# Kernel optimization log

Hardware: AMD Instinct MI355X
Metric: run time of the kernel (lower is better)

## Reference

```python
import jax, jax.numpy as jnp
import numpy as np

L = 12      # n_layers
C = 768     # n_embd = dim = dim_att
H = 12      # heads
N = 64      # head_size_a
FF = 2688   # dim_ffn = int(768*3.5//32*32)
P = 2       # patch_size
INCH = 4
IMG = 32
NCLS = 1000
FREQ = 256
HC = C // 2  # conv stem channels (dim//2)
B = 32
D_MIX = 32
D_DEC = 64
LNX_EPS = 1e-5 * 8.0 ** 2  # GroupNorm eps with head_size_divisor=8


def _ln(x, w=None, b=None, eps=1e-5):
    m = x.mean(-1, keepdims=True)
    v = x.var(-1, keepdims=True)
    xh = (x - m) * jax.lax.rsqrt(v + eps)
    if w is not None:
        xh = xh * w + b
    return xh


def _shift(x):  # RWKV token shift: prepend zero row, drop last
    return jnp.pad(x, ((0, 0), (1, 0), (0, 0)))[:, :-1]


def _gn_img(x, w, b, groups=32, eps=1e-5):
    Bb, Ch, Hh, Ww = x.shape
    xg = x.reshape(Bb, groups, Ch // groups, Hh, Ww)
    m = xg.mean((2, 3, 4), keepdims=True)
    v = xg.var((2, 3, 4), keepdims=True)
    xg = (xg - m) * jax.lax.rsqrt(v + eps)
    return xg.reshape(Bb, Ch, Hh, Ww) * w[None, :, None, None] + b[None, :, None, None]


def _conv5(x, w, b):
    y = jax.lax.conv_general_dilated(x, w, (1, 1), ((2, 2), (2, 2)),
                                     dimension_numbers=('NCHW', 'OIHW', 'NCHW'))
    return y + b[None, :, None, None]


def _wkv(r, k, v, w, u):
    # r,k,v,w: (B,T,H,N); u: (H,N). S[b,h,i,j]: key i -> value j.
    def step(S, inp):
        rt, kt, vt, wt = inp  # each (B,H,N)
        kv = kt[..., :, None] * vt[..., None, :]           # (B,H,N,N)
        y = jnp.einsum('bhi,bhij->bhj', rt, S + u[None, :, :, None] * kv)
        S = wt[..., :, None] * S + kv
        return S, y
    S0 = jnp.zeros((r.shape[0], H, N, N), r.dtype)
    seq = tuple(jnp.moveaxis(a, 1, 0) for a in (r, k, v, w))
    _, ys = jax.lax.scan(step, S0, seq)
    return jnp.moveaxis(ys, 0, 1)  # (B,T,H,N)


def _timemix(x, p):
    Bb, Tt, _ = x.shape
    xx = _shift(x) - x
    xxx = x + xx * p['maa'][0]
    mix = jnp.tanh(xxx @ p['tm_w1']).reshape(Bb, Tt, 5, D_MIX)
    m = jnp.einsum('btfd,fdc->fbtc', mix, p['tm_w2'])  # (5,B,T,C): mw,mk,mv,mr,mg
    xw = x + xx * (p['maa'][1] + m[0])
    xk = x + xx * (p['maa'][2] + m[1])
    xv = x + xx * (p['maa'][3] + m[2])
    xr = x + xx * (p['maa'][4] + m[3])
    xg = x + xx * (p['maa'][5] + m[4])
    r = (xr @ p['r_w'].T).reshape(Bb, Tt, H, N)
    k = (xk @ p['k_w'].T).reshape(Bb, Tt, H, N)
    v = (xv @ p['v_w'].T).reshape(Bb, Tt, H, N)
    g = jax.nn.silu(xg @ p['g_w'].T)
    ww = p['td'] + jnp.tanh(xw @ p['td_w1']) @ p['td_w2']
    w = jnp.exp(-jnp.exp(ww)).reshape(Bb, Tt, H, N)
    y = _wkv(r, k, v, w, p['faaaa'])  # (B,T,H,N)
    mn = y.mean(-1, keepdims=True)
    vr = y.var(-1, keepdims=True)
    y = ((y - mn) * jax.lax.rsqrt(vr + LNX_EPS)).reshape(Bb, Tt, C) * p['lnx_w'] + p['lnx_b']
    return (y * g) @ p['o_w'].T


def _chanmix(x, p):
    xx = _shift(x) - x
    xk = x + xx * p['fmaa'][0]
    xr = x + xx * p['fmaa'][1]
    k = jnp.square(jax.nn.relu(xk @ p['fk_w'].T))
    return jax.nn.sigmoid(xr @ p['fr_w'].T) * (k @ p['fv_w'].T)


def _forward(x, t, y, c1_w, c1_b, gn1_w, gn1_b, c2_w, c2_b, gn2_w, gn2_b,
             xe_w, xe_b, te_w1, te_b1, te_w2, te_b2, y_tab, ln0_w, ln0_b,
             ln1_w, ln1_b, ln2_w, ln2_b, att_maa, tm_w1, tm_w2, td, td_w1,
             td_w2, faaaa, r_w, k_w, v_w, o_w, g_w, lnx_w, lnx_b, ffn_maa,
             fk_w, fr_w, fv_w, ada_w, ada_b, fl_ada_w, fl_ada_b, fl_w, fl_b):
    Bb = x.shape[0]
    h = jax.nn.silu(_conv5(x, c1_w, c1_b))
    h = _gn_img(h, gn1_w, gn1_b)
    h = jax.nn.silu(_conv5(h, c2_w, c2_b))
    h = _gn_img(h, gn2_w, gn2_b)
    # patchify: (B,HC,IMG,IMG) -> (B,T,P*P*HC)
    G = IMG // P
    h = h.reshape(Bb, HC, G, P, G, P).transpose(0, 2, 4, 1, 3, 5).reshape(Bb, G * G, HC * P * P)
    xs = h @ xe_w.T + xe_b
    # timestep embedding
    half = FREQ // 2
    freqs = jnp.exp(-jnp.log(10000.0) * jnp.arange(half, dtype=jnp.float32) / half)
    ang = t[:, None] * freqs[None]
    temb = jnp.concatenate([jnp.cos(ang), jnp.sin(ang)], -1)
    temb = jax.nn.silu(temb @ te_w1.T + te_b1) @ te_w2.T + te_b2
    c = temb + y_tab[y]  # adaln_input (B,C)
    for l in range(L):
        ada = jax.nn.silu(c) @ ada_w[l].T + ada_b[l]
        sm, scm, gm, sp, scp, gp = jnp.split(ada, 6, axis=1)
        if l == 0:
            xs = _ln(xs, ln0_w, ln0_b)
        p = dict(maa=att_maa[l], tm_w1=tm_w1[l], tm_w2=tm_w2[l], td=td[l],
                 td_w1=td_w1[l], td_w2=td_w2[l], faaaa=faaaa[l], r_w=r_w[l],
                 k_w=k_w[l], v_w=v_w[l], o_w=o_w[l], g_w=g_w[l], lnx_w=lnx_w[l],
                 lnx_b=lnx_b[l], fmaa=ffn_maa[l], fk_w=fk_w[l], fr_w=fr_w[l],
                 fv_w=fv_w[l])
        hmod = _ln(xs, ln1_w[l], ln1_b[l]) * (1 + scm[:, None, :]) + sm[:, None, :]
        xs = xs + gm[:, None, :] * _timemix(hmod, p)
        hmod = _ln(xs, ln2_w[l], ln2_b[l]) * (1 + scp[:, None, :]) + sp[:, None, :]
        xs = xs + gp[:, None, :] * _chanmix(hmod, p)
    ada = jax.nn.silu(c) @ fl_ada_w.T + fl_ada_b
    sh, sc = jnp.split(ada, 2, axis=1)
    out = (_ln(xs, eps=1e-6) * (1 + sc[:, None, :]) + sh[:, None, :]) @ fl_w.T + fl_b
    G = IMG // P
    out = out.reshape(Bb, G, G, P, P, INCH)
    out = jnp.einsum('nhwpqc->nchpwq', out).reshape(Bb, INCH, IMG, IMG)
    return out


def setup_inputs() -> dict:
    key = jax.random.key(0)
    ks = iter(jax.random.split(key, 64))
    def rn(shape, s=0.02):
        return (jax.random.normal(next(ks), shape) * s).astype(jnp.float32)
    inp = {}
    inp['x'] = jax.random.normal(next(ks), (B, INCH, IMG, IMG), jnp.float32)
    inp['t'] = jax.random.uniform(next(ks), (B,), jnp.float32) * 1000.0
    inp['y'] = jax.random.randint(next(ks), (B,), 0, NCLS)
    inp['c1_w'] = rn((HC, INCH, 5, 5), 0.05); inp['c1_b'] = jnp.zeros(HC)
    inp['gn1_w'] = jnp.ones(HC); inp['gn1_b'] = jnp.zeros(HC)
    inp['c2_w'] = rn((HC, HC, 5, 5), 0.02); inp['c2_b'] = jnp.zeros(HC)
    inp['gn2_w'] = jnp.ones(HC); inp['gn2_b'] = jnp.zeros(HC)
    inp['xe_w'] = rn((C, P * P * HC)); inp['xe_b'] = jnp.zeros(C)
    inp['te_w1'] = rn((C, FREQ)); inp['te_b1'] = jnp.zeros(C)
    inp['te_w2'] = rn((C, C)); inp['te_b2'] = jnp.zeros(C)
    inp['y_tab'] = rn((NCLS + 1, C))
    inp['ln0_w'] = jnp.ones(C); inp['ln0_b'] = jnp.zeros(C)
    inp['ln1_w'] = jnp.ones((L, C)); inp['ln1_b'] = jnp.zeros((L, C))
    inp['ln2_w'] = jnp.ones((L, C)); inp['ln2_b'] = jnp.zeros((L, C))
    inp['att_maa'] = jax.random.uniform(next(ks), (L, 6, C), jnp.float32)
    inp['tm_w1'] = rn((L, C, 5 * D_MIX), 0.01)
    inp['tm_w2'] = rn((L, 5, D_MIX, C), 0.01)
    inp['td'] = rn((L, C), 0.5) - 3.0
    inp['td_w1'] = rn((L, C, D_DEC), 0.01)
    inp['td_w2'] = rn((L, D_DEC, C), 0.01)
    inp['faaaa'] = rn((L, H, N), 0.1)
    for nm in ('r_w', 'k_w', 'v_w', 'o_w', 'g_w'):
        inp[nm] = rn((L, C, C))
    inp['lnx_w'] = jnp.ones((L, C)); inp['lnx_b'] = jnp.zeros((L, C))
    inp['ffn_maa'] = jax.random.uniform(next(ks), (L, 2, C), jnp.float32)
    inp['fk_w'] = rn((L, FF, C)); inp['fr_w'] = rn((L, C, C)); inp['fv_w'] = rn((L, C, FF))
    inp['ada_w'] = rn((L, 6 * C, C)); inp['ada_b'] = jnp.zeros((L, 6 * C))
    inp['fl_ada_w'] = rn((2 * C, C)); inp['fl_ada_b'] = jnp.zeros(2 * C)
    inp['fl_w'] = rn((P * P * INCH, C)); inp['fl_b'] = jnp.zeros(P * P * INCH)
    return inp


def reference(x, t, y, c1_w, c1_b, gn1_w, gn1_b, c2_w, c2_b, gn2_w, gn2_b,
              xe_w, xe_b, te_w1, te_b1, te_w2, te_b2, y_tab, ln0_w, ln0_b,
              ln1_w, ln1_b, ln2_w, ln2_b, att_maa, tm_w1, tm_w2, td, td_w1,
              td_w2, faaaa, r_w, k_w, v_w, o_w, g_w, lnx_w, lnx_b, ffn_maa,
              fk_w, fr_w, fv_w, ada_w, ada_b, fl_ada_w, fl_ada_b, fl_w, fl_b):
    return _forward(x, t, y, c1_w, c1_b, gn1_w, gn1_b, c2_w, c2_b, gn2_w, gn2_b,
                    xe_w, xe_b, te_w1, te_b1, te_w2, te_b2, y_tab, ln0_w, ln0_b,
                    ln1_w, ln1_b, ln2_w, ln2_b, att_maa, tm_w1, tm_w2, td, td_w1,
                    td_w2, faaaa, r_w, k_w, v_w, o_w, g_w, lnx_w, lnx_b, ffn_maa,
                    fk_w, fr_w, fv_w, ada_w, ada_b, fl_ada_w, fl_ada_b, fl_w, fl_b)
```

## Files before the change

kernel.cpp:

```cpp
#include <hip/hip_runtime.h>
#include <math.h>


typedef short  s16x8 __attribute__((ext_vector_type(8)));
typedef float  f32x4 __attribute__((ext_vector_type(4)));
typedef __attribute__((address_space(1))) const void as1_cv;
typedef __attribute__((address_space(3))) void as3_v;

#define GLDS16(gp, lp) __builtin_amdgcn_global_load_lds( \
    (as1_cv*)(unsigned long long)(const void*)(gp), \
    (as3_v*)(unsigned int)(unsigned long long)(void*)(lp), 16, 0, 0)

static __device__ __forceinline__ float sigf(float x){ return 1.f/(1.f+expf(-x)); }
static __device__ __forceinline__ unsigned short f2b(float x){
  unsigned int u = __builtin_bit_cast(unsigned int, x);
  unsigned int r = (u + 0x7FFFu + ((u >> 16) & 1u)) >> 16;
  return (unsigned short)r;
}
static __device__ __forceinline__ float b2f(unsigned short h){
  unsigned int u = ((unsigned int)h)<<16; return __builtin_bit_cast(float,u);
}

static const size_t O_XS    = 0ull;
static const size_t O_HMOD  = 6291456ull;
// ... 106 lines not shown
template<int EPI>
__global__ __launch_bounds__(256) void bgemm_k(
    const unsigned short* __restrict__ A, const unsigned short* __restrict__ B,
    void* __restrict__ Cv, const float* __restrict__ bias,
    const float* __restrict__ p1, const void* __restrict__ p2, int pstride,
    int M, int N, int K)
{
  __shared__ __align__(16) unsigned short As[128][64];
  __shared__ __align__(16) unsigned short Bs[128][64];
  const int tid = threadIdx.x;
  const int w = tid >> 6, lane = tid & 63;
  const int row0 = blockIdx.y * 128, col0 = blockIdx.x * 128;
  const int wr = w >> 1, wc = w & 1;
  const int l15 = lane & 15, l4 = lane >> 4;
  const int kkc = ((lane & 7) ^ (lane >> 3)) * 8;
  f32x4 acc[4][4] = {};
  for (int k0 = 0; k0 < K; k0 += 64) {
    #pragma unroll
    for (int i = 0; i < 4; i++) {
      const int rb = i*32 + w*8;
      const int r  = rb + (lane >> 3);
      GLDS16(A + (size_t)(row0 + r)*K + k0 + kkc, &As[rb][0]);
      GLDS16(B + (size_t)(col0 + r)*K + k0 + kkc, &Bs[rb][0]);
    }
    __syncthreads();
    #pragma unroll
    for (int ks = 0; ks < 2; ks++) {
      s16x8 af[4], bf[4];
      #pragma unroll
      for (int m = 0; m < 4; m++) {
        const int r = wr*64 + m*16 + l15;
        const int sl = (ks*4 + l4) ^ (r & 7);
        af[m] = *reinterpret_cast<const s16x8*>(&As[r][sl*8]);
      }
      #pragma unroll
      for (int n = 0; n < 4; n++) {
        const int r = wc*64 + n*16 + l15;
        const int sl = (ks*4 + l4) ^ (r & 7);
        bf[n] = *reinterpret_cast<const s16x8*>(&Bs[r][sl*8]);
      }
      #pragma unroll
      for (int m = 0; m < 4; m++)
        #pragma unroll
        for (int n = 0; n < 4; n++)
          acc[m][n] = __builtin_amdgcn_mfma_f32_16x16x32_bf16(af[m], bf[n], acc[m][n], 0, 0, 0);
    }
    __syncthreads();
  }
  float* Cf = (float*)Cv; unsigned short* Ch = (unsigned short*)Cv;
  const unsigned short* p2h = (const unsigned short*)p2;
  #pragma unroll
  for (int m = 0; m < 4; m++) {
    const int rbase = row0 + wr*64 + m*16 + (l4<<2);
    #pragma unroll
    for (int n = 0; n < 4; n++) {
      const int c = col0 + wc*64 + n*16 + l15;
      if (c >= N) continue;
      #pragma unroll
      for (int q = 0; q < 4; q++) {
        const int r = rbase + q;
        const int bb = r >> 8;
        float v = acc[m][n][q];
        const size_t idx = (size_t)r*N + c;
        if (EPI==BEPI_F32)            Cf[idx] = v;
        else if (EPI==BEPI_BIAS_F32)  Cf[idx] = v + bias[c];
        else if (EPI==BEPI_SILU_F32)  Cf[idx] = v*sigf(v);
        else if (EPI==BEPI_SIG_F32)   Cf[idx] = sigf(v);
        else if (EPI==BEPI_RELU2_BF16){ float t=fmaxf(v,0.f); Ch[idx] = f2b(t*t); }
        else if (EPI==BEPI_RES_GM)    Cf[idx] += p1[(size_t)bb*pstride + c]*v;
        else if (EPI==BEPI_RES_GP16)  Cf[idx] += p1[(size_t)bb*pstride + c]*(b2f(p2h[idx])*v);
        else if (EPI==BEPI_TANH_BF16) Ch[idx] = f2b(tanhf(v));
        else if (EPI==BEPI_WDEC_F32)  Cf[idx] = expf(-expf(v + p1[c]));
      }
    }
  }
}

#define BGEMM(EPI,A16,B16,Cp,bias,p1,p2,ps,M,N,K) \
  bgemm_k<EPI><<<dim3(((N)+127)/128,(M)/128),dim3(256),0,stream>>>( \
    (const unsigned short*)(A16),(const unsigned short*)(B16),(void*)(Cp),(bias),(p1),(p2),(ps),(M),(N),(K))

struct BGrp { const unsigned short* A; const unsigned short* B; void* C;
              int epi; int N; int gx; };
struct BGrp5 { BGrp g[5]; };

__global__ __launch_bounds__(256) void bgemm_grp_k(BGrp5 G, int M, int K)
{
  const BGrp gr = G.g[blockIdx.z];
  if ((int)blockIdx.x >= gr.gx) return;
  __shared__ __align__(16) unsigned short As[128][64];
  __shared__ __align__(16) unsigned short Bs[128][64];
  const int tid = threadIdx.x;
  const int w = tid >> 6, lane = tid & 63;
  const int row0 = blockIdx.y * 128, col0 = blockIdx.x * 128;
  const int wr = w >> 1, wc = w & 1;
  const int l15 = lane & 15, l4 = lane >> 4;
  const int kkc = ((lane & 7) ^ (lane >> 3)) * 8;
  const int N = gr.N;
  f32x4 acc[4][4] = {};
  for (int k0 = 0; k0 < K; k0 += 64) {
    #pragma unroll
    for (int i = 0; i < 4; i++) {
      const int rb = i*32 + w*8;
      const int r  = rb + (lane >> 3);
      GLDS16(gr.A + (size_t)(row0 + r)*K + k0 + kkc, &As[rb][0]);
      GLDS16(gr.B + (size_t)(col0 + r)*K + k0 + kkc, &Bs[rb][0]);
    }
    __syncthreads();
    #pragma unroll
    for (int ks = 0; ks < 2; ks++) {
      s16x8 af[4], bf[4];
      #pragma unroll
      for (int m = 0; m < 4; m++) {
        const int r = wr*64 + m*16 + l15;
        const int sl = (ks*4 + l4) ^ (r & 7);
        af[m] = *reinterpret_cast<const s16x8*>(&As[r][sl*8]);
      }
      #pragma unroll
      for (int n = 0; n < 4; n++) {
        const int r = wc*64 + n*16 + l15;
        const int sl = (ks*4 + l4) ^ (r & 7);
        bf[n] = *reinterpret_cast<const s16x8*>(&Bs[r][sl*8]);
      }
      #pragma unroll
      for (int m = 0; m < 4; m++)
        #pragma unroll
        for (int n = 0; n < 4; n++)
          acc[m][n] = __builtin_amdgcn_mfma_f32_16x16x32_bf16(af[m], bf[n], acc[m][n], 0, 0, 0);
    }
    __syncthreads();
  }
  float* Cf = (float*)gr.C; unsigned short* Ch = (unsigned short*)gr.C;
  #pragma unroll
  for (int m = 0; m < 4; m++) {
    const int rbase = row0 + wr*64 + m*16 + (l4<<2);
    #pragma unroll
    for (int n = 0; n < 4; n++) {
      const int c = col0 + wc*64 + n*16 + l15;
      #pragma unroll
      for (int q = 0; q < 4; q++) {
        const int r = rbase + q;
        float v = acc[m][n][q];
        const size_t idx = (size_t)r*N + c;
        switch (gr.epi) {
          case 0: Cf[idx] = v; break;
          case 1: Cf[idx] = v*sigf(v); break;
          case 3: { float t=fmaxf(v,0.f); Ch[idx] = f2b(t*t); } break;
          case 4: Ch[idx] = f2b(v); break;
          case 5: Ch[idx] = f2b(v*sigf(v)); break;
          case 6: Ch[idx] = f2b(tanhf(v)); break;
          default: Ch[idx] = f2b(sigf(v)); break;
        }
      }
    }
  }
}

__global__ __launch_bounds__(256) void conv1_k(
    const float* __restrict__ x, const float* __restrict__ w,
    const float* __restrict__ bias, float* __restrict__ out)
{
  const int blk = blockIdx.x; const int bb = blk / 384; const int oc = blk % 384;
  __shared__ __align__(16) float sIn[4*1296];
  __shared__ __align__(16) float sW[100];
  const int tid = threadIdx.x;
  for (int idx=tid; idx<4*1296; idx+=256){
    int ic = idx/1296; int rem = idx - ic*1296;
    int yy = rem/36, xx = rem - yy*36;
    int gy = yy-2, gx = xx-2;
    float v = 0.f;
    if ((unsigned)gy < 32u && (unsigned)gx < 32u)
      v = x[(((size_t)bb*4+ic)*32+gy)*32+gx];
    sIn[idx]=v;
  }
  if (tid < 100) sW[tid] = w[(size_t)oc*100 + tid];
  __syncthreads();
  const float bv = bias[oc];
  #pragma unroll
  for (int i=0;i<4;i++){
    int p = tid + 256*i; int py=p>>5, px=p&31;
    int pb = py*36+px;
    float acc = bv;
    #pragma unroll
    for (int ic=0;ic<4;ic++)
      #pragma unroll
      for (int ky=0;ky<5;ky++)
        #pragma unroll
        for (int kx=0;kx<5;kx++)
          acc = fmaf(sIn[ic*1296 + pb + ky*36+kx], sW[ic*25+ky*5+kx], acc);
    out[((size_t)(bb*384+oc))*1024 + p] = acc*sigf(acc);
  }
}

__global__ __launch_bounds__(256) void gn_stats_nchw_k(
    const float* __restrict__ h, float* __restrict__ stats)
{
  const int blk = blockIdx.x;
  const size_t base = (size_t)blk*12288;
  const int tid = threadIdx.x;
  float s=0.f, s2=0.f;
  for (int idx=tid; idx<12288; idx+=256){ float v=h[base+idx]; s+=v; s2=fmaf(v,v,s2); }
  #pragma unroll
  for (int mask=32; mask>=1; mask>>=1){ s += __shfl_xor(s,mask); s2 += __shfl_xor(s2,mask); }
  __shared__ float ps[8];
  if ((tid&63)==0){ ps[tid>>6]=s; ps[4+(tid>>6)]=s2; }
  __syncthreads();
  if (tid==0){
    s = ps[0]+ps[1]+ps[2]+ps[3]; s2 = ps[4]+ps[5]+ps[6]+ps[7];
    float mean = s*(1.f/12288.f);
    float var  = s2*(1.f/12288.f) - mean*mean;
    stats[blk*2] = mean; stats[blk*2+1] = rsqrtf(var + 1e-5f);
  }
}

__global__ void zero16_k(unsigned short* __restrict__ p)
{
  size_t i = ((size_t)blockIdx.x*256 + threadIdx.x)*8;
  *reinterpret_cast<uint4*>(p + i) = make_uint4(0u,0u,0u,0u);
}

__global__ __launch_bounds__(256) void pad_apply_k(
    const float* __restrict__ img1, const float* __restrict__ stats,
    const float* __restrict__ w, const float* __restrict__ bgn,
    unsigned short* __restrict__ pad)
{
  __shared__ float t[8][33];
  const int b = blockIdx.x >> 5, y = blockIdx.x & 31;
  const int tid = threadIdx.x;
  for (int ic0 = 0; ic0 < 384; ic0 += 8) {
    const int icr = tid >> 5, xr = tid & 31;
    t[icr][xr] = img1[(((size_t)b*384 + ic0+icr)*32 + y)*32 + xr];
    __syncthreads();
    const int xw_ = tid >> 3, icw = tid & 7;
// ... 107 lines not shown
  if ((tid&63)==0){ ps[tid>>6]=s; ps[4+(tid>>6)]=s2; }
  __syncthreads();
  if (tid==0){
    s = ps[0]+ps[1]+ps[2]+ps[3]; s2 = ps[4]+ps[5]+ps[6]+ps[7];
    float mean = s*(1.f/12288.f);
    float var  = s2*(1.f/12288.f) - mean*mean;
    stats[(b*32+g)*2] = mean; stats[(b*32+g)*2+1] = rsqrtf(var + 1e-5f);
  }
}

__global__ void patchify_gn_k(const unsigned short* __restrict__ h, const float* __restrict__ stats,
                              const float* __restrict__ w, const float* __restrict__ bgn,
                              unsigned short* __restrict__ pm)
{
  int idx = blockIdx.x*256 + threadIdx.x;
  int row = idx/1536, f = idx - row*1536;
  int c = f>>2; int p=(f>>1)&1; int q=f&1;
  int bb=row>>8; int tok=row&255; int gh=tok>>4, gw=tok&15;
  int pix = (gh*2+p)*32 + gw*2+q;
  int g = c / 12;
  float mean = stats[(bb*32+g)*2], rstd = stats[(bb*32+g)*2+1];
  float v = (b2f(h[((size_t)bb*1024 + pix)*384 + c]) - mean)*rstd*w[c] + bgn[c];
  pm[idx] = f2b(v);
}

__global__ void temb_in_k(const float* __restrict__ t, float* __restrict__ out)
{
  int bb = blockIdx.x; int i = threadIdx.x;
  float fr = expf(-logf(10000.f) * (float)i / 128.f);
  float ang = t[bb]*fr;
  out[bb*256+i]     = cosf(ang);
  out[bb*256+128+i] = sinf(ang);
}

__global__ void siluc_k(const float* __restrict__ t2, const float* __restrict__ ytab,
                        const int* __restrict__ y, float* __restrict__ sc)
{
  int bb = blockIdx.x; int tid = threadIdx.x;
  int cls = y[bb];
  for (int c=tid; c<768; c+=256){
    float v = t2[bb*768+c] + ytab[(size_t)cls*768+c];
    sc[bb*768+c] = v*sigf(v);
  }
}

__global__ __launch_bounds__(256) void ln_mod_k(
    const float* __restrict__ in, float* __restrict__ out,
    const float* __restrict__ w, const float* __restrict__ b,
    const float* __restrict__ mod, int mstride, int sh_off, int sc_off, float eps)
{
  const int m = blockIdx.x; const int tid = threadIdx.x;
  const size_t base = (size_t)m*768;
  float v0=in[base+tid], v1=in[base+tid+256], v2=in[base+tid+512];
  float s = v0+v1+v2;
  float s2 = fmaf(v0,v0,fmaf(v1,v1,v2*v2));
  #pragma unroll
  for (int mask=32; mask>=1; mask>>=1){ s += __shfl_xor(s,mask); s2 += __shfl_xor(s2,mask); }
  __shared__ float ps[8];
  if ((tid&63)==0){ ps[tid>>6]=s; ps[4+(tid>>6)]=s2; }
  __syncthreads();
  s = ps[0]+ps[1]+ps[2]+ps[3]; s2 = ps[4]+ps[5]+ps[6]+ps[7];
  const float mean = s*(1.f/768.f);
  const float var  = s2*(1.f/768.f) - mean*mean;
  const float rstd = rsqrtf(var + eps);
  const int bb = m >> 8;
  #pragma unroll
  for (int k=0;k<3;k++){
    const int c = tid + k*256;
    float v = (k==0)?v0:((k==1)?v1:v2);
    float xh = (v-mean)*rstd;
    if (w) xh = fmaf(xh, w[c], b[c]);
    if (mod){
      float scv = mod[(size_t)bb*mstride + sc_off + c];
      float shv = mod[(size_t)bb*mstride + sh_off + c];
      xh = fmaf(xh, 1.f+scv, shv);
    }
    out[base+c] = xh;
  }
}

__global__ __launch_bounds__(256) void ln_shift_tm_k(
    const float* __restrict__ xs, const float* __restrict__ w, const float* __restrict__ b,
    const float* __restrict__ mod, const float* __restrict__ maa0,
    float* __restrict__ hmod, float* __restrict__ xx, unsigned short* __restrict__ xxx16)
{
  const int m = blockIdx.x, tid = threadIdx.x;
  const size_t base = (size_t)m*768;
  const int t = m & 255, bb = m >> 8;
  float c0=xs[base+tid], c1=xs[base+tid+256], c2=xs[base+tid+512];
  float p0=0.f,p1=0.f,p2=0.f;
  if (t) { p0=xs[base-768+tid]; p1=xs[base-512+tid]; p2=xs[base-256+tid]; }
  float sc_=c0+c1+c2, sc2=fmaf(c0,c0,fmaf(c1,c1,c2*c2));
  float sp_=p0+p1+p2, sp2=fmaf(p0,p0,fmaf(p1,p1,p2*p2));
  #pragma unroll
  for (int mask=32; mask>=1; mask>>=1){
    sc_+=__shfl_xor(sc_,mask); sc2+=__shfl_xor(sc2,mask);
    sp_+=__shfl_xor(sp_,mask); sp2+=__shfl_xor(sp2,mask);
  }
  __shared__ float ps[16];
  if ((tid&63)==0){ int wv=tid>>6; ps[wv]=sc_; ps[4+wv]=sc2; ps[8+wv]=sp_; ps[12+wv]=sp2; }
  __syncthreads();
  sc_=ps[0]+ps[1]+ps[2]+ps[3]; sc2=ps[4]+ps[5]+ps[6]+ps[7];
  sp_=ps[8]+ps[9]+ps[10]+ps[11]; sp2=ps[12]+ps[13]+ps[14]+ps[15];
  const float mc = sc_*(1.f/768.f), rc = rsqrtf(sc2*(1.f/768.f)-mc*mc + 1e-5f);
  const float mp = sp_*(1.f/768.f), rp = rsqrtf(sp2*(1.f/768.f)-mp*mp + 1e-5f);
  #pragma unroll
  for (int k=0;k<3;k++){
    const int c = tid + k*256;
    const float scv = mod[(size_t)bb*55296 + 768 + c];
    const float shv = mod[(size_t)bb*55296 + c];
    float cv = (k==0)?c0:((k==1)?c1:c2);
    float h = fmaf((cv-mc)*rc, w[c], b[c]);
    h = fmaf(h, 1.f+scv, shv);
    float pv = 0.f;
    if (t) {
      float pk = (k==0)?p0:((k==1)?p1:p2);
      pv = fmaf((pk-mp)*rp, w[c], b[c]);
      pv = fmaf(pv, 1.f+scv, shv);
    }
    const float d = pv - h;
    hmod[base+c] = h;
    xx[base+c] = d;
    xxx16[base+c] = f2b(fmaf(d, maa0[c], h));
  }
}

__global__ __launch_bounds__(256) void ln_shift_cm_k(
    const float* __restrict__ xs, const float* __restrict__ w, const float* __restrict__ b,
    const float* __restrict__ mod, const float* __restrict__ fmaa,
    unsigned short* __restrict__ xk16, unsigned short* __restrict__ xr16)
{
  const int m = blockIdx.x, tid = threadIdx.x;
  const size_t base = (size_t)m*768;
  const int t = m & 255, bb = m >> 8;
  float c0=xs[base+tid], c1=xs[base+tid+256], c2=xs[base+tid+512];
  float p0=0.f,p1=0.f,p2=0.f;
  if (t) { p0=xs[base-768+tid]; p1=xs[base-512+tid]; p2=xs[base-256+tid]; }
  float sc_=c0+c1+c2, sc2=fmaf(c0,c0,fmaf(c1,c1,c2*c2));
  float sp_=p0+p1+p2, sp2=fmaf(p0,p0,fmaf(p1,p1,p2*p2));
  #pragma unroll
  for (int mask=32; mask>=1; mask>>=1){
    sc_+=__shfl_xor(sc_,mask); sc2+=__shfl_xor(sc2,mask);
    sp_+=__shfl_xor(sp_,mask); sp2+=__shfl_xor(sp2,mask);
  }
  __shared__ float ps[16];
  if ((tid&63)==0){ int wv=tid>>6; ps[wv]=sc_; ps[4+wv]=sc2; ps[8+wv]=sp_; ps[12+wv]=sp2; }
  __syncthreads();
  sc_=ps[0]+ps[1]+ps[2]+ps[3]; sc2=ps[4]+ps[5]+ps[6]+ps[7];
  sp_=ps[8]+ps[9]+ps[10]+ps[11]; sp2=ps[12]+ps[13]+ps[14]+ps[15];
  const float mc = sc_*(1.f/768.f), rc = rsqrtf(sc2*(1.f/768.f)-mc*mc + 1e-5f);
  const float mp = sp_*(1.f/768.f), rp = rsqrtf(sp2*(1.f/768.f)-mp*mp + 1e-5f);
  #pragma unroll
  for (int k=0;k<3;k++){
    const int c = tid + k*256;
    const float scv = mod[(size_t)bb*55296 + 3072 + c];
    const float shv = mod[(size_t)bb*55296 + 2304 + c];
    float cv = (k==0)?c0:((k==1)?c1:c2);
    float h = fmaf((cv-mc)*rc, w[c], b[c]);
    h = fmaf(h, 1.f+scv, shv);
    float pv = 0.f;
    if (t) {
      float pk = (k==0)?p0:((k==1)?p1:p2);
      pv = fmaf((pk-mp)*rp, w[c], b[c]);
      pv = fmaf(pv, 1.f+scv, shv);
    }
    const float d = pv - h;
    xk16[base+c] = f2b(fmaf(d, fmaa[c], h));
    xr16[base+c] = f2b(fmaf(d, fmaa[768+c], h));
  }
}

__global__ __launch_bounds__(256) void five_mix_k(
    const unsigned short* __restrict__ mix16, const float* __restrict__ w2,
    const float* __restrict__ hmod, const float* __restrict__ xx,
    const float* __restrict__ maa15,
    unsigned short* __restrict__ xw, unsigned short* __restrict__ xk,
    unsigned short* __restrict__ xv, unsigned short* __restrict__ xr,
    unsigned short* __restrict__ xg)
{
  __shared__ __align__(16) float smix[8][160];
  const int m0 = blockIdx.x * 8;
  const int tid = threadIdx.x;
  for (int idx=tid; idx<8*160; idx+=256){
    int r = idx/160, d = idx - r*160;
    smix[r][d] = b2f(mix16[(size_t)(m0+r)*160 + d]);
  }
  __syncthreads();
  #pragma unroll 1
  for (int cc=0; cc<3; cc++){
    const int c = tid + cc*256;
    float hv[8], xv_[8];
    #pragma unroll
    for (int r=0;r<8;r++){ size_t id=(size_t)(m0+r)*768+c; hv[r]=hmod[id]; xv_[r]=xx[id]; }
    #pragma unroll 1
    for (int f=0; f<5; f++){
      float acc[8];
      const float base = maa15[f*768 + c];
      #pragma unroll
      for (int r=0;r<8;r++) acc[r]=base;
      #pragma unroll 1
      for (int d4=0; d4<8; d4++){
        float wv[4];
        #pragma unroll
        for (int q=0;q<4;q++) wv[q] = w2[(size_t)(f*32+d4*4+q)*768 + c];
        #pragma unroll
        for (int r=0;r<8;r++){
          const float4 mv = *reinterpret_cast<const float4*>(&smix[r][f*32+d4*4]);
          acc[r] = fmaf(mv.x,wv[0],fmaf(mv.y,wv[1],fmaf(mv.z,wv[2],fmaf(mv.w,wv[3],acc[r]))));
        }
      }
      #pragma unroll
      for (int r=0;r<8;r++){
        float val = fmaf(xv_[r], acc[r], hv[r]);
        size_t id = (size_t)(m0+r)*768+c;
        if (f==0) xw[id]=f2b(val);
        else if (f==1) xk[id]=f2b(val);
        else if (f==2) xv[id]=f2b(val);
        else if (f==3) xr[id]=f2b(val);
        else           xg[id]=f2b(val);
      }
    }
  }
}

__global__ __launch_bounds__(256) void wkv_k(
    const unsigned short* __restrict__ rg, const unsigned short* __restrict__ kg,
    const unsigned short* __restrict__ vg, const float* __restrict__ wg,
    const unsigned short* __restrict__ gg, const float* __restrict__ u,
    const float* __restrict__ lnxw, const float* __restrict__ lnxb,
    unsigned short* __restrict__ out16)
{
  const int bh = blockIdx.x; const int b = bh/12, h = bh%12;
  const int tid = threadIdx.x;
  const int w = tid >> 6, lane = tid & 63;
  const int l4 = lane >> 4, l15 = lane & 15;
  __shared__ __align__(16) unsigned short r16s[32][64], k16s[32][64], v16s[32][64], g16s[32][64];
  __shared__ __align__(16) float wds[32][64];
  __shared__ __align__(16) float Wl[33][64];
  __shared__ __align__(16) unsigned short rr16[32][64], kk16[32][64];
  __shared__ __align__(16) unsigned short kk2T[64][32], vT[64][32];
  __shared__ __align__(16) unsigned short S16T[64][64];
  __shared__ __align__(16) unsigned short A16[32][32];
  __shared__ float diag[32], ypsum[32][4], ypsq[32][4];

  reinterpret_cast<uint4*>(&S16T[0][0])[tid] = make_uint4(0,0,0,0);
  reinterpret_cast<uint4*>(&S16T[0][0])[256+tid] = make_uint4(0,0,0,0);

  const float u_lane = u[h*64 + lane];
  const int jj = w*16 + l15;
  const float lw = lnxw[h*64 + jj], lb = lnxb[h*64 + jj];
  const size_t gb = (size_t)(b*256)*768 + h*64;

  const int st_t = tid >> 3, st_i = (tid & 7) * 8;
  uint4 pr, pk, pv, pg; float4 pw0, pw1;

#define WKV_LOADC(c_) { \
    const size_t tb = gb + (size_t)((c_)*32 + st_t)*768 + st_i; \
    pr = *reinterpret_cast<const uint4*>(rg + tb); \
    pk = *reinterpret_cast<const uint4*>(kg + tb); \
    pv = *reinterpret_cast<const uint4*>(vg + tb); \
    pg = *reinterpret_cast<const uint4*>(gg + tb); \
    pw0 = *reinterpret_cast<const float4*>(wg + tb); \
    pw1 = *reinterpret_cast<const float4*>(wg + tb + 4); }
#define WKV_STAGE() { \
    *reinterpret_cast<uint4*>(&r16s[st_t][st_i]) = pr; \
    *reinterpret_cast<uint4*>(&k16s[st_t][st_i]) = pk; \
    *reinterpret_cast<uint4*>(&v16s[st_t][st_i]) = pv; \
    *reinterpret_cast<uint4*>(&g16s[st_t][st_i]) = pg; \
    *reinterpret_cast<float4*>(&wds[st_t][st_i]) = pw0; \
    *reinterpret_cast<float4*>(&wds[st_t][st_i+4]) = pw1; }

  f32x4 S_acc[4] = {};

  WKV_LOADC(0);
  WKV_STAGE();
  __syncthreads();

  #pragma unroll 1
  for (int c = 0; c < 8; ++c) {
    if (w == 0) {
      float wv[32];
      #pragma unroll
      for (int t=0;t<32;t++) wv[t] = wds[t][lane];
      float P = 1.f;
      Wl[0][lane] = 1.f;
      #pragma unroll
      for (int t=0;t<32;t++){ P *= wv[t]; Wl[t+1][lane] = P; }
    }
    __syncthreads();
    {
      const int t = st_t, i0 = st_i;
      s16x8 rv = *reinterpret_cast<const s16x8*>(&r16s[t][i0]);
      s16x8 kv = *reinterpret_cast<const s16x8*>(&k16s[t][i0]);
      s16x8 vv = *reinterpret_cast<const s16x8*>(&v16s[t][i0]);
      float4 wa0 = *reinterpret_cast<const float4*>(&Wl[t][i0]);
// ... 97 lines not shown
    #pragma unroll
    for (int m=0;m<2;m++)
      #pragma unroll
      for (int q=0;q<4;q++){
        float s1 = Y[m][q], s2 = s1*s1;
        #pragma unroll
        for (int mask=8; mask>=1; mask>>=1){ s1 += __shfl_xor(s1,mask); s2 += __shfl_xor(s2,mask); }
        if (l15==0){ const int t = m*16 + l4*4 + q; ypsum[t][w]=s1; ypsq[t][w]=s2; }
      }
    __syncthreads();
    #pragma unroll
    for (int m=0;m<2;m++)
      #pragma unroll
      for (int q=0;q<4;q++){
        const int t = m*16 + l4*4 + q;
        float s1 = ypsum[t][0]+ypsum[t][1]+ypsum[t][2]+ypsum[t][3];
        float s2 = ypsq[t][0]+ypsq[t][1]+ypsq[t][2]+ypsq[t][3];
        float mean = s1*(1.f/64.f);
        float var  = s2*(1.f/64.f) - mean*mean;
        float xh = (Y[m][q]-mean)*rsqrtf(var + 6.4e-4f);
        float o = fmaf(xh, lw, lb) * b2f(g16s[t][jj]);
        out16[gb + (size_t)(c*32+t)*768 + jj] = f2b(o);
      }
    if (c < 7) {
      __syncthreads();
      WKV_STAGE();
      __syncthreads();
    }
  }
#undef WKV_LOADC
#undef WKV_STAGE
}

__global__ void unpatch_k(const float* __restrict__ po, float* __restrict__ out)
{
  int idx = blockIdx.x*256 + threadIdx.x;
  int xq=idx&31; int yy=(idx>>5)&31; int ch=(idx>>10)&3; int bb=idx>>12;
  int gh=yy>>1, p=yy&1, gw=xq>>1, q=xq&1;
  out[idx] = po[((size_t)(bb*256+gh*16+gw))*16 + p*8+q*4+ch];
}

__global__ void f2b_k(const float* __restrict__ s, unsigned short* __restrict__ d)
{
  size_t i = ((size_t)blockIdx.x*256 + threadIdx.x)*8;
  float4 a = *reinterpret_cast<const float4*>(s+i);
  float4 b = *reinterpret_cast<const float4*>(s+i+4);
  s16x8 o;
  o[0]=(short)f2b(a.x); o[1]=(short)f2b(a.y); o[2]=(short)f2b(a.z); o[3]=(short)f2b(a.w);
  o[4]=(short)f2b(b.x); o[5]=(short)f2b(b.y); o[6]=(short)f2b(b.z); o[7]=(short)f2b(b.w);
  *reinterpret_cast<s16x8*>(d + i) = o;
}

__global__ void f2bw_layer_k(
    const float* __restrict__ r_, const float* __restrict__ k_, const float* __restrict__ v_,
    const float* __restrict__ o_, const float* __restrict__ g_, const float* __restrict__ fr_,
    const float* __restrict__ fk_, const float* __restrict__ fv_,
    const float* __restrict__ tm1, const float* __restrict__ td1, const float* __restrict__ td2,
    unsigned short* __restrict__ dst)
{
  if (blockIdx.x < 3744) {
    size_t i = ((size_t)blockIdx.x*256 + threadIdx.x)*8;
    const float* s; size_t off;
    if (i < 3538944) {
      unsigned seg = (unsigned)(i / 589824u); off = i - (size_t)seg*589824u;
      s = seg==0?r_:seg==1?k_:seg==2?v_:seg==3?o_:seg==4?g_:fr_;
    } else if (i < 5603328) { s = fk_; off = i - 3538944; }
    else                    { s = fv_; off = i - 5603328; }
    float4 a = *reinterpret_cast<const float4*>(s+off);
    float4 b = *reinterpret_cast<const float4*>(s+off+4);
    s16x8 o;
    o[0]=(short)f2b(a.x); o[1]=(short)f2b(a.y); o[2]=(short)f2b(a.z); o[3]=(short)f2b(a.w);
    o[4]=(short)f2b(b.x); o[5]=(short)f2b(b.y); o[6]=(short)f2b(b.z); o[7]=(short)f2b(b.w);
    *reinterpret_cast<s16x8*>(dst + i) = o;
  } else {
    int idx = (blockIdx.x-3744)*256 + threadIdx.x;
    unsigned short* rp = dst + 7667712;
    if (idx < 196608) {
      int n = idx/768, k = idx - n*768;
      rp[idx] = (n<160) ? f2b(tm1[(size_t)k*160 + n]) : (unsigned short)0;
    } else if (idx < 294912) {
      int i = idx-196608; int n = i/768, k = i - n*768;
      rp[idx] = (n<64) ? f2b(td1[(size_t)k*64 + n]) : (unsigned short)0;
    } else {
      int i = idx-294912; int n = i/128, kk = i & 127;
      rp[idx] = (kk<64) ? f2b(td2[(size_t)kk*768 + n]) : (unsigned short)0;
    }
  }
}

extern "C" void kernel_launch(void* const* d_in, const int* in_sizes, int n_in,
                              void* d_out, int out_size, void* d_ws, size_t ws_size,
                              hipStream_t stream)
{
  const float* x_in  = (const float*)d_in[0];
  const float* t_in  = (const float*)d_in[1];
  const int*   y_in  = (const int*)  d_in[2];
  const float* c1w   = (const float*)d_in[3];
  const float* c1b   = (const float*)d_in[4];
  const float* gn1w  = (const float*)d_in[5];
  const float* gn1b  = (const float*)d_in[6];
  const float* c2w   = (const float*)d_in[7];
  const float* c2b   = (const float*)d_in[8];
  const float* gn2w  = (const float*)d_in[9];
  const float* gn2b  = (const float*)d_in[10];
  const float* xew   = (const float*)d_in[11];
  const float* xeb   = (const float*)d_in[12];
  const float* tew1  = (const float*)d_in[13];
  const float* teb1  = (const float*)d_in[14];
  const float* tew2  = (const float*)d_in[15];
  const float* teb2  = (const float*)d_in[16];
  const float* ytab  = (const float*)d_in[17];
  const float* ln0w  = (const float*)d_in[18];
  const float* ln0b  = (const float*)d_in[19];
  const float* ln1w  = (const float*)d_in[20];
  const float* ln1b  = (const float*)d_in[21];
  const float* ln2w  = (const float*)d_in[22];
  const float* ln2b  = (const float*)d_in[23];
  const float* amaa  = (const float*)d_in[24];
  const float* tmw1  = (const float*)d_in[25];
  const float* tmw2  = (const float*)d_in[26];
  const float* tdv   = (const float*)d_in[27];
  const float* tdw1  = (const float*)d_in[28];
  const float* tdw2  = (const float*)d_in[29];
  const float* faa   = (const float*)d_in[30];
  const float* rw    = (const float*)d_in[31];
  const float* kw    = (const float*)d_in[32];
  const float* vw    = (const float*)d_in[33];
  const float* ow    = (const float*)d_in[34];
  const float* gw    = (const float*)d_in[35];
  const float* lnxw  = (const float*)d_in[36];
  const float* lnxb  = (const float*)d_in[37];
  const float* fmaa  = (const float*)d_in[38];
  const float* fkw   = (const float*)d_in[39];
  const float* frw   = (const float*)d_in[40];
  const float* fvw   = (const float*)d_in[41];
  const float* adaw  = (const float*)d_in[42];
  const float* adab  = (const float*)d_in[43];
  const float* flaw  = (const float*)d_in[44];
  const float* flab  = (const float*)d_in[45];
  const float* flw   = (const float*)d_in[46];
  const float* flb   = (const float*)d_in[47];

  float* Wf = (float*)d_ws;
  float* xs   = Wf+O_XS;   float* hmod = Wf+O_HMOD;
  float* ada  = Wf+O_ADA;  float* fla  = Wf+O_FLA;
  float* t2   = Wf+O_T2;   float* sc   = Wf+O_SC;
  float* ti   = Wf+O_TI;   float* t1   = Wf+O_T1;
  float* st1  = Wf+O_ST1;  float* st2  = Wf+O_ST2;
  unsigned short* xew16 = (unsigned short*)(Wf+O_XEW16);
  unsigned short* wl16  = (unsigned short*)(Wf+O_WL16);
  float* big = Wf+O_BIG;
  float* xxb  = big+L_XX;
  float* wd   = big+L_WD;
  unsigned short* rb16  = (unsigned short*)(big+L_XXX);
  unsigned short* kb16  = (unsigned short*)(big+L_KB);
  unsigned short* vb16  = (unsigned short*)(big+L_VB);
  unsigned short* gb16  = (unsigned short*)(big+L_GB);
  unsigned short* xw16  = (unsigned short*)(big+L_XW);
  unsigned short* xxx16 = (unsigned short*)(big+L_XXX);
  unsigned short* mixb16= (unsigned short*)(big+L_MIXB);
  unsigned short* wt16  = (unsigned short*)(big+L_WT);
  unsigned short* xk16 = (unsigned short*)(big+L_XK16);
  unsigned short* xv16 = (unsigned short*)(big+L_XV16);
  unsigned short* xr16 = (unsigned short*)(big+L_XR16);
  unsigned short* xg16 = (unsigned short*)(big+L_XG16);
  unsigned short* gnh16 = (unsigned short*)(big+L_GNH16);
  unsigned short* kbig16 = (unsigned short*)(big+L_KBIG16);
  float* img1 = big+S_IMG1;
  unsigned short* img2_16 = (unsigned short*)(big+S_IMG2);
  unsigned short* pad16  = (unsigned short*)(big+S_PAD16);
  unsigned short* wtap16 = (unsigned short*)(big+S_WTAP16);
  unsigned short* pm16   = (unsigned short*)(big+S_PM16);
  float* pout = big+L_MIXB;
  unsigned short* dr  = wl16;
  unsigned short* dk  = wl16 + 589824;
  unsigned short* dv  = wl16 + 1179648;
  unsigned short* do_ = wl16 + 1769472;
  unsigned short* dg  = wl16 + 2359296;
  unsigned short* dfr = wl16 + 2949120;
  unsigned short* dfk = wl16 + 3538944;
  unsigned short* dfv = wl16 + 5603328;
  unsigned short* dtm1t = wl16 + 7667712;
  unsigned short* dtd1t = wl16 + 7864320;
  unsigned short* dtd2t = wl16 + 7962624;

  conv1_k<<<dim3(32*384),dim3(256),0,stream>>>(x_in, c1w, c1b, img1);
  gn_stats_nchw_k<<<dim3(1024),dim3(256),0,stream>>>(img1, st1);
  zero16_k<<<dim3(7776),dim3(256),0,stream>>>(pad16);
  pad_apply_k<<<dim3(1024),dim3(256),0,stream>>>(img1, st1, gn1w, gn1b, pad16);
  wrepack_k<<<dim3(384),dim3(256),0,stream>>>(c2w, wtap16);
  conv2m_k<<<dim3(768),dim3(256),0,stream>>>(pad16, wtap16, c2b, img2_16);
  gn_stats_nhwc_k<<<dim3(1024),dim3(256),0,stream>>>(img2_16, st2);
  patchify_gn_k<<<dim3(49152),dim3(256),0,stream>>>(img2_16, st2, gn2w, gn2b, pm16);
  f2b_k<<<dim3(576),dim3(256),0,stream>>>(xew, xew16);
  BGEMM(BEPI_BIAS_F32, pm16, xew16, xs, xeb, nullptr,nullptr,0, 8192,768,1536);

  temb_in_k<<<dim3(32),dim3(128),0,stream>>>(t_in, ti);
  GEMM(EPI_SILU,true, ti, tew1, t1, teb1, 32,768,256);
  GEMM(EPI_NONE,true, t1, tew2, t2, teb2, 32,768,768);
  siluc_k<<<dim3(32),dim3(256),0,stream>>>(t2, ytab, y_in, sc);
  GEMM(EPI_NONE,true, sc, adaw, ada, adab, 32,55296,768);
  GEMM(EPI_NONE,true, sc, flaw, fla, flab, 32,1536,768);

  ln_mod_k<<<dim3(8192),dim3(256),0,stream>>>(xs, xs, ln0w, ln0b, nullptr, 0,0,0, 1e-5f);

  for (int l=0; l<12; l++){
    const float* adal = ada + (size_t)l*4608;
    f2bw_layer_k<<<dim3(5280),dim3(256),0,stream>>>(
        rw+(size_t)l*589824, kw+(size_t)l*589824, vw+(size_t)l*589824,
        ow+(size_t)l*589824, gw+(size_t)l*589824, frw+(size_t)l*589824,
        fkw+(size_t)l*2064384, fvw+(size_t)l*2064384,
        tmw1+(size_t)l*122880, tdw1+(size_t)l*49152, tdw2+(size_t)l*49152, wl16);
    ln_shift_tm_k<<<dim3(8192),dim3(256),0,stream>>>(
        xs, ln1w+(size_t)l*768, ln1b+(size_t)l*768, adal, amaa+(size_t)l*4608,
        hmod, xxb, xxx16);
    BGEMM(BEPI_TANH_BF16, xxx16, dtm1t, mixb16, nullptr,nullptr,nullptr,0, 8192,160,768);
    five_mix_k<<<dim3(1024),dim3(256),0,stream>>>(mixb16, tmw2+(size_t)l*122880, hmod, xxb,
                                                  amaa+(size_t)l*4608+768, xw16,xk16,xv16,xr16,xg16);
    {
      BGrp5 G;
      G.g[0].A=xr16; G.g[0].B=dr;    G.g[0].C=rb16; G.g[0].epi=4; G.g[0].N=768; G.g[0].gx=6;
      G.g[1].A=xk16; G.g[1].B=dk;    G.g[1].C=kb16; G.g[1].epi=4; G.g[1].N=768; G.g[1].gx=6;
      G.g[2].A=xv16; G.g[2].B=dv;    G.g[2].C=vb16; G.g[2].epi=4; G.g[2].N=768; G.g[2].gx=6;
      G.g[3].A=xg16; G.g[3].B=dg;    G.g[3].C=gb16; G.g[3].epi=5; G.g[3].N=768; G.g[3].gx=6;
      G.g[4].A=xw16; G.g[4].B=dtd1t; G.g[4].C=wt16; G.g[4].epi=6; G.g[4].N=128; G.g[4].gx=1;
      bgemm_grp_k<<<dim3(6,64,5),dim3(256),0,stream>>>(G, 8192, 768);
    }
    BGEMM(BEPI_WDEC_F32, wt16, dtd2t, wd, nullptr, tdv+(size_t)l*768, nullptr,0, 8192,768,128);
    wkv_k<<<dim3(384),dim3(256),0,stream>>>(rb16, kb16, vb16, wd, gb16, faa+(size_t)l*768,
                                            lnxw+(size_t)l*768, lnxb+(size_t)l*768, gnh16);
    BGEMM(BEPI_RES_GM, gnh16, do_, xs, nullptr, adal+1536, nullptr, 55296, 8192,768,768);
    ln_shift_cm_k<<<dim3(8192),dim3(256),0,stream>>>(
        xs, ln2w+(size_t)l*768, ln2b+(size_t)l*768, adal, fmaa+(size_t)l*1536, xk16, xr16);
    {
      BGrp5 G;
      G.g[0].A=xk16; G.g[0].B=dfk; G.g[0].C=kbig16; G.g[0].epi=3; G.g[0].N=2688; G.g[0].gx=21;
      G.g[1].A=xr16; G.g[1].B=dfr; G.g[1].C=gb16;   G.g[1].epi=7; G.g[1].N=768;  G.g[1].gx=6;
      G.g[2]=G.g[1]; G.g[3]=G.g[1]; G.g[4]=G.g[1];
      bgemm_grp_k<<<dim3(21,64,2),dim3(256),0,stream>>>(G, 8192, 768);
    }
    BGEMM(BEPI_RES_GP16, kbig16, dfv, xs, nullptr, adal+3840, gb16, 55296, 8192,768,2688);
  }

  ln_mod_k<<<dim3(8192),dim3(256),0,stream>>>(xs, hmod, nullptr, nullptr, fla, 1536, 0, 768, 1e-6f);
  GEMM(EPI_NONE,true, hmod, flw, pout, flb, 8192,16,768);
  unpatch_k<<<dim3(512),dim3(256),0,stream>>>(pout, (float*)d_out);
}
```

Measured before the change: 9.043 ms.

## Store timemix intermediates as bf16 and split decay LoRA out of grouped GEMM

hmod and xx are now written and read in bf16 instead of fp32, roughly halving their memory traffic between ln_shift_tm_k and five_mix_k. five_mix_k processes 16 rows per block instead of 8, so each w2 weight load is reused across more rows. The decay LoRA first GEMM is removed from the grouped projection GEMM and run as a standalone N=64 GEMM, and its second stage now uses K=64 instead of a zero-padded 128, which shrinks the repacked weights and the f2bw grid. The bf16 intermediates lower precision, and the larger per-thread register arrays may reduce occupancy.

```diff
diff --git a/kernel.cpp b/kernel.cpp
--- a/kernel.cpp
+++ b/kernel.cpp
@@ -212,9 +212,9 @@
 
 struct BGrp { const unsigned short* A; const unsigned short* B; void* C;
               int epi; int N; int gx; };
-struct BGrp5 { BGrp g[5]; };
-
-__global__ __launch_bounds__(256) void bgemm_grp_k(BGrp5 G, int M, int K)
+struct BGrp4 { BGrp g[4]; };
+
+__global__ __launch_bounds__(256) void bgemm_grp_k(BGrp4 G, int M, int K)
 {
   const BGrp gr = G.g[blockIdx.z];
   if ((int)blockIdx.x >= gr.gx) return;
@@ -278,7 +278,6 @@
           case 3: { float t=fmaxf(v,0.f); Ch[idx] = f2b(t*t); } break;
           case 4: Ch[idx] = f2b(v); break;
           case 5: Ch[idx] = f2b(v*sigf(v)); break;
-          case 6: Ch[idx] = f2b(tanhf(v)); break;
           default: Ch[idx] = f2b(sigf(v)); break;
         }
       }
@@ -552,7 +551,8 @@
 __global__ __launch_bounds__(256) void ln_shift_tm_k(
     const float* __restrict__ xs, const float* __restrict__ w, const float* __restrict__ b,
     const float* __restrict__ mod, const float* __restrict__ maa0,
-    float* __restrict__ hmod, float* __restrict__ xx, unsigned short* __restrict__ xxx16)
+    unsigned short* __restrict__ hmod16, unsigned short* __restrict__ xx16,
+    unsigned short* __restrict__ xxx16)
 {
   const int m = blockIdx.x, tid = threadIdx.x;
   const size_t base = (size_t)m*768;
@@ -589,8 +589,8 @@
       pv = fmaf(pv, 1.f+scv, shv);
     }
     const float d = pv - h;
-    hmod[base+c] = h;
-    xx[base+c] = d;
+    hmod16[base+c] = f2b(h);
+    xx16[base+c] = f2b(d);
     xxx16[base+c] = f2b(fmaf(d, maa0[c], h));
   }
 }
@@ -642,16 +642,16 @@
 
 __global__ __launch_bounds__(256) void five_mix_k(
     const unsigned short* __restrict__ mix16, const float* __restrict__ w2,
-    const float* __restrict__ hmod, const float* __restrict__ xx,
+    const unsigned short* __restrict__ hmod16, const unsigned short* __restrict__ xx16,
     const float* __restrict__ maa15,
     unsigned short* __restrict__ xw, unsigned short* __restrict__ xk,
     unsigned short* __restrict__ xv, unsigned short* __restrict__ xr,
     unsigned short* __restrict__ xg)
 {
-  __shared__ __align__(16) float smix[8][160];
-  const int m0 = blockIdx.x * 8;
+  __shared__ __align__(16) float smix[16][160];
+  const int m0 = blockIdx.x * 16;
   const int tid = threadIdx.x;
-  for (int idx=tid; idx<8*160; idx+=256){
+  for (int idx=tid; idx<16*160; idx+=256){
     int r = idx/160, d = idx - r*160;
     smix[r][d] = b2f(mix16[(size_t)(m0+r)*160 + d]);
   }
@@ -659,28 +659,31 @@
   #pragma unroll 1
   for (int cc=0; cc<3; cc++){
     const int c = tid + cc*256;
-    float hv[8], xv_[8];
-    #pragma unroll
-    for (int r=0;r<8;r++){ size_t id=(size_t)(m0+r)*768+c; hv[r]=hmod[id]; xv_[r]=xx[id]; }
+    float hv[16], xv_[16];
+    #pragma unroll
+    for (int r=0;r<16;r++){
+      size_t id=(size_t)(m0+r)*768+c;
+      hv[r]=b2f(hmod16[id]); xv_[r]=b2f(xx16[id]);
+    }
     #pragma unroll 1
     for (int f=0; f<5; f++){
-      float acc[8];
+      float acc[16];
       const float base = maa15[f*768 + c];
       #pragma unroll
-      for (int r=0;r<8;r++) acc[r]=base;
+      for (int r=0;r<16;r++) acc[r]=base;
       #pragma unroll 1
       for (int d4=0; d4<8; d4++){
         float wv[4];
         #pragma unroll
         for (int q=0;q<4;q++) wv[q] = w2[(size_t)(f*32+d4*4+q)*768 + c];
         #pragma unroll
-        for (int r=0;r<8;r++){
+        for (int r=0;r<16;r++){
           const float4 mv = *reinterpret_cast<const float4*>(&smix[r][f*32+d4*4]);
           acc[r] = fmaf(mv.x,wv[0],fmaf(mv.y,wv[1],fmaf(mv.z,wv[2],fmaf(mv.w,wv[3],acc[r]))));
         }
       }
       #pragma unroll
-      for (int r=0;r<8;r++){
+      for (int r=0;r<16;r++){
         float val = fmaf(xv_[r], acc[r], hv[r]);
         size_t id = (size_t)(m0+r)*768+c;
         if (f==0) xw[id]=f2b(val);
@@ -944,8 +947,8 @@
       int i = idx-196608; int n = i/768, k = i - n*768;
       rp[idx] = (n<64) ? f2b(td1[(size_t)k*64 + n]) : (unsigned short)0;
     } else {
-      int i = idx-294912; int n = i/128, kk = i & 127;
-      rp[idx] = (kk<64) ? f2b(td2[(size_t)kk*768 + n]) : (unsigned short)0;
+      int i = idx-294912; int n = i/64, k = i - n*64;
+      rp[idx] = f2b(td2[(size_t)k*768 + n]);
     }
   }
 }
@@ -1004,16 +1007,17 @@
   const float* flb   = (const float*)d_in[47];
 
   float* Wf = (float*)d_ws;
-  float* xs   = Wf+O_XS;   float* hmod = Wf+O_HMOD;
+  float* xs   = Wf+O_XS;   float* hmodf = Wf+O_HMOD;
   float* ada  = Wf+O_ADA;  float* fla  = Wf+O_FLA;
   float* t2   = Wf+O_T2;   float* sc   = Wf+O_SC;
   float* ti   = Wf+O_TI;   float* t1   = Wf+O_T1;
   float* st1  = Wf+O_ST1;  float* st2  = Wf+O_ST2;
   unsigned short* xew16 = (unsigned short*)(Wf+O_XEW16);
   unsigned short* wl16  = (unsigned short*)(Wf+O_WL16);
+  unsigned short* hmod16 = (unsigned short*)(Wf+O_HMOD);
   float* big = Wf+O_BIG;
-  float* xxb  = big+L_XX;
   float* wd   = big+L_WD;
+  unsigned short* xx16  = (unsigned short*)(big+L_XX);
   unsigned short* rb16  = (unsigned short*)(big+L_XXX);
   unsigned short* kb16  = (unsigned short*)(big+L_KB);
   unsigned short* vb16  = (unsigned short*)(big+L_VB);
@@ -1068,43 +1072,43 @@
 
   for (int l=0; l<12; l++){
     const float* adal = ada + (size_t)l*4608;
-    f2bw_layer_k<<<dim3(5280),dim3(256),0,stream>>>(
+    f2bw_layer_k<<<dim3(5088),dim3(256),0,stream>>>(
         rw+(size_t)l*589824, kw+(size_t)l*589824, vw+(size_t)l*589824,
         ow+(size_t)l*589824, gw+(size_t)l*589824, frw+(size_t)l*589824,
         fkw+(size_t)l*2064384, fvw+(size_t)l*2064384,
         tmw1+(size_t)l*122880, tdw1+(size_t)l*49152, tdw2+(size_t)l*49152, wl16);
     ln_shift_tm_k<<<dim3(8192),dim3(256),0,stream>>>(
         xs, ln1w+(size_t)l*768, ln1b+(size_t)l*768, adal, amaa+(size_t)l*4608,
-        hmod, xxb, xxx16);
+        hmod16, xx16, xxx16);
     BGEMM(BEPI_TANH_BF16, xxx16, dtm1t, mixb16, nullptr,nullptr,nullptr,0, 8192,160,768);
-    five_mix_k<<<dim3(1024),dim3(256),0,stream>>>(mixb16, tmw2+(size_t)l*122880, hmod, xxb,
-                                                  amaa+(size_t)l*4608+768, xw16,xk16,xv16,xr16,xg16);
+    five_mix_k<<<dim3(512),dim3(256),0,stream>>>(mixb16, tmw2+(size_t)l*122880, hmod16, xx16,
+                                                 amaa+(size_t)l*4608+768, xw16,xk16,xv16,xr16,xg16);
+    BGEMM(BEPI_TANH_BF16, xw16, dtd1t, wt16, nullptr,nullptr,nullptr,0, 8192,64,768);
+    BGEMM(BEPI_WDEC_F32, wt16, dtd2t, wd, nullptr, tdv+(size_t)l*768, nullptr,0, 8192,768,64);
     {
-      BGrp5 G;
-      G.g[0].A=xr16; G.g[0].B=dr;    G.g[0].C=rb16; G.g[0].epi=4; G.g[0].N=768; G.g[0].gx=6;
-      G.g[1].A=xk16; G.g[1].B=dk;    G.g[1].C=kb16; G.g[1].epi=4; G.g[1].N=768; G.g[1].gx=6;
-      G.g[2].A=xv16; G.g[2].B=dv;    G.g[2].C=vb16; G.g[2].epi=4; G.g[2].N=768; G.g[2].gx=6;
-      G.g[3].A=xg16; G.g[3].B=dg;    G.g[3].C=gb16; G.g[3].epi=5; G.g[3].N=768; G.g[3].gx=6;
-      G.g[4].A=xw16; G.g[4].B=dtd1t; G.g[4].C=wt16; G.g[4].epi=6; G.g[4].N=128; G.g[4].gx=1;
-      bgemm_grp_k<<<dim3(6,64,5),dim3(256),0,stream>>>(G, 8192, 768);
-    }
-    BGEMM(BEPI_WDEC_F32, wt16, dtd2t, wd, nullptr, tdv+(size_t)l*768, nullptr,0, 8192,768,128);
+      BGrp4 G;
+      G.g[0].A=xr16; G.g[0].B=dr; G.g[0].C=rb16; G.g[0].epi=4; G.g[0].N=768; G.g[0].gx=6;
+      G.g[1].A=xk16; G.g[1].B=dk; G.g[1].C=kb16; G.g[1].epi=4; G.g[1].N=768; G.g[1].gx=6;
+      G.g[2].A=xv16; G.g[2].B=dv; G.g[2].C=vb16; G.g[2].epi=4; G.g[2].N=768; G.g[2].gx=6;
+      G.g[3].A=xg16; G.g[3].B=dg; G.g[3].C=gb16; G.g[3].epi=5; G.g[3].N=768; G.g[3].gx=6;
+      bgemm_grp_k<<<dim3(6,64,4),dim3(256),0,stream>>>(G, 8192, 768);
+    }
     wkv_k<<<dim3(384),dim3(256),0,stream>>>(rb16, kb16, vb16, wd, gb16, faa+(size_t)l*768,
                                             lnxw+(size_t)l*768, lnxb+(size_t)l*768, gnh16);
     BGEMM(BEPI_RES_GM, gnh16, do_, xs, nullptr, adal+1536, nullptr, 55296, 8192,768,768);
     ln_shift_cm_k<<<dim3(8192),dim3(256),0,stream>>>(
         xs, ln2w+(size_t)l*768, ln2b+(size_t)l*768, adal, fmaa+(size_t)l*1536, xk16, xr16);
     {
-      BGrp5 G;
+      BGrp4 G;
       G.g[0].A=xk16; G.g[0].B=dfk; G.g[0].C=kbig16; G.g[0].epi=3; G.g[0].N=2688; G.g[0].gx=21;
       G.g[1].A=xr16; G.g[1].B=dfr; G.g[1].C=gb16;   G.g[1].epi=7; G.g[1].N=768;  G.g[1].gx=6;
-      G.g[2]=G.g[1]; G.g[3]=G.g[1]; G.g[4]=G.g[1];
+      G.g[2]=G.g[1]; G.g[3]=G.g[1];
       bgemm_grp_k<<<dim3(21,64,2),dim3(256),0,stream>>>(G, 8192, 768);
     }
     BGEMM(BEPI_RES_GP16, kbig16, dfv, xs, nullptr, adal+3840, gb16, 55296, 8192,768,2688);
   }
 
-  ln_mod_k<<<dim3(8192),dim3(256),0,stream>>>(xs, hmod, nullptr, nullptr, fla, 1536, 0, 768, 1e-6f);
-  GEMM(EPI_NONE,true, hmod, flw, pout, flb, 8192,16,768);
+  ln_mod_k<<<dim3(8192),dim3(256),0,stream>>>(xs, hmodf, nullptr, nullptr, fla, 1536, 0, 768, 1e-6f);
+  GEMM(EPI_NONE,true, hmodf, flw, pout, flb, 8192,16,768);
   unpatch_k<<<dim3(512),dim3(256),0,stream>>>(pout, (float*)d_out);
 }
```

Result: faster. 8.233 ms (median of 3 runs) (-9.0%).
